# Performance work log

Hardware: AMD Instinct MI355X
Metric: run time of the kernel (lower is better)

## Reference

```python
import jax, jax.numpy as jnp
import numpy as np

GROUP_SIZE = 128  # QuantizationConfig default


def setup_inputs() -> dict:
    key = jax.random.key(0)
    k0, k1, k2, k3 = jax.random.split(key, 4)
    B, IN, OUT = 32, 4096, 16384
    NG = IN // GROUP_SIZE  # 32 groups
    x = jax.random.normal(k0, (B, IN), dtype=jnp.float16)
    # int8 symmetric-quantized weights in [-127, 127]
    qweight = jax.random.randint(k1, (OUT, IN), -127, 128, dtype=jnp.int8)
    # per-(out_channel, group) fp16 scales; small positive values as produced by absmax/127
    scales = (jax.random.uniform(k2, (OUT, NG), dtype=jnp.float16) * jnp.float16(0.01)
              + jnp.float16(1e-3))
    bias = jax.random.normal(k3, (OUT,), dtype=jnp.float16) * jnp.float16(0.01)
    return {"x": x, "qweight": qweight, "scales": scales, "bias": bias}


def reference(x, qweight, scales, bias):
    # QuantizedLinear._forward_grouped, sym=True, in_features % group_size == 0 path.
    OUT, IN = qweight.shape
    NG = IN // GROUP_SIZE
    # dequantize: [OUT, NG, G] * [OUT, NG, 1] -> [OUT, IN], all in fp16
    w_deq = (qweight.astype(jnp.float16).reshape(OUT, NG, GROUP_SIZE)
             * scales[:, :, None]).reshape(OUT, IN)
    # F.linear(x, w_deq) = x @ w_deq.T, then + bias
    out = jnp.dot(x, w_deq.T) + bias
    return out
```

## Files before the change

### kernel.cpp

```cpp
#include <hip/hip_runtime.h>

typedef __attribute__((ext_vector_type(8))) short short8;
typedef __attribute__((ext_vector_type(4))) float f32x4;
typedef __attribute__((ext_vector_type(4))) int   i32x4;

#define IN_F   4096
#define OUT_F  16384
#define NG     32
#define BK     64
#define NCH    32

static __device__ __forceinline__ short f2bf(float f) {
    union { float f; unsigned u; } c; c.f = f;
    unsigned u = c.u;
    u += 0x7FFF + ((u >> 16) & 1);
    return (short)(u >> 16);
}

static __device__ __forceinline__ short i2bf(int v) {
    union { float f; unsigned u; } c; c.f = (float)v;
    return (short)(c.u >> 16);
}

__global__ __launch_bounds__(256)
void xconv_kernel(const float* __restrict__ x, unsigned short* __restrict__ xT) {
    const int g   = blockIdx.x * 256 + threadIdx.x;
    const int t   = g >> 7;
    const int rem = g & 127;
    const int h   = rem >> 6;
    const int ln  = rem & 63;
    const int l15 = ln >> 2;
    const int l4  = ln & 3;
    const float* src = x + (size_t)(16 * h + l15) * IN_F + t * 32 + l4 * 8;
    f32x4 a = *(const f32x4*)src;
    f32x4 b = *(const f32x4*)(src + 4);
    short8 o;
#pragma unroll
    for (int j = 0; j < 4; ++j) { o[j] = f2bf(a[j]); o[j + 4] = f2bf(b[j]); }
    *(short8*)(xT + (size_t)g * 8) = o;
}

__global__ __launch_bounds__(512, 4)
void qlin_kernel(const unsigned short* __restrict__ xT,
                 const int*   __restrict__ qw,
                 const float* __restrict__ scales,
                 const float* __restrict__ bias,
                 float*       __restrict__ out)
{
    __shared__ int lqw[2][3][32][BK];

    const int tid  = threadIdx.x;
    const int wv   = tid >> 6;
    const int lane = tid & 63;
    const int l15  = lane & 15;
    const int l4   = lane >> 4;
    const int wk   = wv >> 2;
    const int wm   = (wv >> 1) & 1;
    const int wn   = wv & 1;
    const int widx = wv & 3;
    const int col0 = blockIdx.x * 32;

    const int rowB = 16 * wn + l15;
    const int swzB = (rowB & 7) << 4;

    auto STAGE = [&](int c, int sl) {
        const size_t kbase = (size_t)wk * 2048 + (size_t)c * BK;
#pragma unroll
        for (int i = 0; i < 2; ++i) {
            const int p   = widx * 2 + i;
            const int row = 4 * p + (lane >> 4);
            const int byt = ((lane & 15) * 16) ^ ((row & 7) << 4);
            const char* src = (const char*)(qw + (size_t)(col0 + row) * IN_F + kbase) + byt;
            __builtin_amdgcn_global_load_lds(
                (const __attribute__((address_space(1))) unsigned int*)src,
                (__attribute__((address_space(3))) unsigned int*)&lqw[wk][sl][4 * p][0],
                16, 0, 0);
        }
    };

    const unsigned short* xgrp = xT + (size_t)(l15 * 4 + l4) * 8 + (size_t)wm * 512;
    short8 xa[2][2];
    auto XLOAD = [&](int c, int par) {
        const int t = wk * 64 + c * 2;
        xa[par][0] = *(const short8*)(xgrp + (size_t)t * 1024);
        xa[par][1] = *(const short8*)(xgrp + (size_t)(t + 1) * 1024);
    };

    const float* scr = scales + (size_t)(col0 + rowB) * NG + wk * 16;
    f32x4 sc4[4];
#pragma unroll
    for (int j = 0; j < 4; ++j) sc4[j] = *(const f32x4*)(scr + 4 * j);

    f32x4 acc = {0.f, 0.f, 0.f, 0.f};

    auto COMPUTE = [&](int c, int sl, int par, float sc) {
        const char* lrow = (const char*)&lqw[wk][sl][rowB][0];
        f32x4 ag = {0.f, 0.f, 0.f, 0.f};
#pragma unroll
        for (int s = 0; s < 2; ++s) {
            const int byte0 = (s * 128 + l4 * 32) ^ swzB;
            i32x4 q0 = *(const i32x4*)(lrow + byte0);
            i32x4 q1 = *(const i32x4*)(lrow + (byte0 ^ 16));
            short8 bfr;
#pragma unroll
            for (int j = 0; j < 4; ++j) { bfr[j] = i2bf(q0[j]); bfr[j + 4] = i2bf(q1[j]); }
            ag = __builtin_amdgcn_mfma_f32_16x16x32_bf16(xa[par][s], bfr, ag, 0, 0, 0);
        }
#pragma unroll
        for (int r = 0; r < 4; ++r) acc[r] += sc * ag[r];
    };

    XLOAD(0, 0);
    XLOAD(1, 1);
    asm volatile("" ::: "memory");
    STAGE(0, 0);
    STAGE(1, 1);
    asm volatile("s_waitcnt vmcnt(2)" ::: "memory");
    __builtin_amdgcn_s_barrier();
    __builtin_amdgcn_sched_barrier(0);

#pragma unroll
    for (int i = 0; i <= 29; ++i) {
        COMPUTE(i, i % 3, i & 1, sc4[(i >> 3)][(i >> 1) & 3]);
        XLOAD(i + 2, i & 1);
        asm volatile("" ::: "memory");
        STAGE(i + 2, (i + 2) % 3);
        asm volatile("s_waitcnt vmcnt(4)" ::: "memory");
        __builtin_amdgcn_s_barrier();
        __builtin_amdgcn_sched_barrier(0);
    }
    COMPUTE(30, 0, 0, sc4[3][3]);
    asm volatile("s_waitcnt vmcnt(0)" ::: "memory");
    __builtin_amdgcn_s_barrier();
    __builtin_amdgcn_sched_barrier(0);
    COMPUTE(31, 1, 1, sc4[3][3]);

    __syncthreads();
    float* red = (float*)&lqw[0][0][0][0];
    *(f32x4*)&red[(size_t)(wv * 64 + lane) * 4] = acc;
    __syncthreads();
    if (wv < 4) {
        const int col = col0 + rowB;
        const float bv = bias[col];
        f32x4 lo = *(const f32x4*)&red[(size_t)(wv * 64 + lane) * 4];
        f32x4 hi = *(const f32x4*)&red[(size_t)((wv + 4) * 64 + lane) * 4];
#pragma unroll
        for (int r = 0; r < 4; ++r)
            out[(size_t)(16 * wm + l4 * 4 + r) * OUT_F + col] = lo[r] + hi[r] + bv;
    }
}

extern "C" void kernel_launch(void* const* d_in, const int* in_sizes, int n_in,
                              void* d_out, int out_size, void* d_ws, size_t ws_size,
                              hipStream_t stream) {
    const float* x      = (const float*)d_in[0];
    const int*   qw     = (const int*)d_in[1];
    const float* scales = (const float*)d_in[2];
    const float* bias   = (const float*)d_in[3];
    float*       out    = (float*)d_out;
    unsigned short* xT  = (unsigned short*)d_ws;

    hipLaunchKernelGGL(xconv_kernel, dim3(64), dim3(256), 0, stream, x, xT);
    hipLaunchKernelGGL(qlin_kernel, dim3(OUT_F / 32), dim3(512), 0, stream,
                       xT, qw, scales, bias, out);
}
```

Measured before the change: 52.61 us.

## Halve block column tile and split K four ways across waves

Each block now covers 16 output columns instead of 32, doubling the grid to 1024 blocks. The four waves per M-half each take a quarter of every 256-wide K chunk, and their partial sums are combined with a four-way LDS reduction. The intent is more blocks for better load balance and more memory-level parallelism while streaming the int32-stored weights. The cost is a larger reduction, strided scale loads, and x reloaded by twice as many blocks.

```diff
diff --git a/kernel.cpp b/kernel.cpp
--- a/kernel.cpp
+++ b/kernel.cpp
@@ -7,8 +7,9 @@
 #define IN_F   4096
 #define OUT_F  16384
 #define NG     32
-#define BK     64
-#define NCH    32
+#define BKI    256
+#define NCH    16
+#define BN     16
 
 static __device__ __forceinline__ short f2bf(float f) {
     union { float f; unsigned u; } c; c.f = f;
@@ -47,33 +48,28 @@
                  const float* __restrict__ bias,
                  float*       __restrict__ out)
 {
-    __shared__ int lqw[2][3][32][BK];
+    __shared__ int lqw[3][BN][BKI];
 
     const int tid  = threadIdx.x;
     const int wv   = tid >> 6;
     const int lane = tid & 63;
     const int l15  = lane & 15;
     const int l4   = lane >> 4;
-    const int wk   = wv >> 2;
-    const int wm   = (wv >> 1) & 1;
-    const int wn   = wv & 1;
-    const int widx = wv & 3;
-    const int col0 = blockIdx.x * 32;
+    const int q    = wv & 3;
+    const int wm   = wv >> 2;
+    const int col0 = blockIdx.x * BN;
 
-    const int rowB = 16 * wn + l15;
-    const int swzB = (rowB & 7) << 4;
+    const int swz = (l15 & 7) << 4;
 
     auto STAGE = [&](int c, int sl) {
-        const size_t kbase = (size_t)wk * 2048 + (size_t)c * BK;
 #pragma unroll
         for (int i = 0; i < 2; ++i) {
-            const int p   = widx * 2 + i;
-            const int row = 4 * p + (lane >> 4);
-            const int byt = ((lane & 15) * 16) ^ ((row & 7) << 4);
-            const char* src = (const char*)(qw + (size_t)(col0 + row) * IN_F + kbase) + byt;
+            const int row = 2 * wv + i;
+            const int byt = (lane * 16) ^ ((row & 7) << 4);
+            const char* src = (const char*)(qw + (size_t)(col0 + row) * IN_F + c * BKI) + byt;
             __builtin_amdgcn_global_load_lds(
                 (const __attribute__((address_space(1))) unsigned int*)src,
-                (__attribute__((address_space(3))) unsigned int*)&lqw[wk][sl][4 * p][0],
+                (__attribute__((address_space(3))) unsigned int*)&lqw[sl][row][0],
                 16, 0, 0);
         }
     };
@@ -81,26 +77,26 @@
     const unsigned short* xgrp = xT + (size_t)(l15 * 4 + l4) * 8 + (size_t)wm * 512;
     short8 xa[2][2];
     auto XLOAD = [&](int c, int par) {
-        const int t = wk * 64 + c * 2;
+        const int t = c * 8 + q * 2;
         xa[par][0] = *(const short8*)(xgrp + (size_t)t * 1024);
         xa[par][1] = *(const short8*)(xgrp + (size_t)(t + 1) * 1024);
     };
 
-    const float* scr = scales + (size_t)(col0 + rowB) * NG + wk * 16;
-    f32x4 sc4[4];
+    const float* scr = scales + (size_t)(col0 + l15) * NG + (q >> 1);
+    float sc_arr[16];
 #pragma unroll
-    for (int j = 0; j < 4; ++j) sc4[j] = *(const f32x4*)(scr + 4 * j);
+    for (int j = 0; j < 16; ++j) sc_arr[j] = scr[2 * j];
 
     f32x4 acc = {0.f, 0.f, 0.f, 0.f};
 
     auto COMPUTE = [&](int c, int sl, int par, float sc) {
-        const char* lrow = (const char*)&lqw[wk][sl][rowB][0];
+        const char* lrow = (const char*)&lqw[sl][l15][0];
         f32x4 ag = {0.f, 0.f, 0.f, 0.f};
 #pragma unroll
         for (int s = 0; s < 2; ++s) {
-            const int byte0 = (s * 128 + l4 * 32) ^ swzB;
-            i32x4 q0 = *(const i32x4*)(lrow + byte0);
-            i32x4 q1 = *(const i32x4*)(lrow + (byte0 ^ 16));
+            const int off = (q * 256 + s * 128 + l4 * 32) ^ swz;
+            i32x4 q0 = *(const i32x4*)(lrow + off);
+            i32x4 q1 = *(const i32x4*)(lrow + (off ^ 16));
             short8 bfr;
 #pragma unroll
             for (int j = 0; j < 4; ++j) { bfr[j] = i2bf(q0[j]); bfr[j + 4] = i2bf(q1[j]); }
@@ -120,8 +116,8 @@
     __builtin_amdgcn_sched_barrier(0);
 
 #pragma unroll
-    for (int i = 0; i <= 29; ++i) {
-        COMPUTE(i, i % 3, i & 1, sc4[(i >> 3)][(i >> 1) & 3]);
+    for (int i = 0; i <= 13; ++i) {
+        COMPUTE(i, i % 3, i & 1, sc_arr[i]);
         XLOAD(i + 2, i & 1);
         asm volatile("" ::: "memory");
         STAGE(i + 2, (i + 2) % 3);
@@ -129,24 +125,29 @@
         __builtin_amdgcn_s_barrier();
         __builtin_amdgcn_sched_barrier(0);
     }
-    COMPUTE(30, 0, 0, sc4[3][3]);
+    COMPUTE(14, 14 % 3, 0, sc_arr[14]);
     asm volatile("s_waitcnt vmcnt(0)" ::: "memory");
     __builtin_amdgcn_s_barrier();
     __builtin_amdgcn_sched_barrier(0);
-    COMPUTE(31, 1, 1, sc4[3][3]);
+    COMPUTE(15, 15 % 3, 1, sc_arr[15]);
 
     __syncthreads();
-    float* red = (float*)&lqw[0][0][0][0];
+    float* red = (float*)&lqw[0][0][0];
     *(f32x4*)&red[(size_t)(wv * 64 + lane) * 4] = acc;
     __syncthreads();
-    if (wv < 4) {
-        const int col = col0 + rowB;
+    if (q == 0) {
+        f32x4 s = *(const f32x4*)&red[(size_t)(wv * 64 + lane) * 4];
+#pragma unroll
+        for (int w = 1; w < 4; ++w) {
+            f32x4 t = *(const f32x4*)&red[(size_t)((wv + w) * 64 + lane) * 4];
+#pragma unroll
+            for (int r = 0; r < 4; ++r) s[r] += t[r];
+        }
+        const int col = col0 + l15;
         const float bv = bias[col];
-        f32x4 lo = *(const f32x4*)&red[(size_t)(wv * 64 + lane) * 4];
-        f32x4 hi = *(const f32x4*)&red[(size_t)((wv + 4) * 64 + lane) * 4];
 #pragma unroll
         for (int r = 0; r < 4; ++r)
-            out[(size_t)(16 * wm + l4 * 4 + r) * OUT_F + col] = lo[r] + hi[r] + bv;
+            out[(size_t)(16 * wm + l4 * 4 + r) * OUT_F + col] = s[r] + bv;
     }
 }
 
@@ -161,6 +162,6 @@
     unsigned short* xT  = (unsigned short*)d_ws;
 
     hipLaunchKernelGGL(xconv_kernel, dim3(64), dim3(256), 0, stream, x, xT);
-    hipLaunchKernelGGL(qlin_kernel, dim3(OUT_F / 32), dim3(512), 0, stream,
+    hipLaunchKernelGGL(qlin_kernel, dim3(OUT_F / BN), dim3(512), 0, stream,
                        xT, qw, scales, bias, out);
 }
```

Result: slower. 72.33 us (+37.5%).
